# Kernel optimization log

Hardware: AMD Instinct MI355X
Metric: run time of the kernel (lower is better)

## Reference

```python
import jax, jax.numpy as jnp
import numpy as np

B, T, C, NH = 4, 2048, 1024, 16
HS = C // NH  # 64


def setup_inputs() -> dict:
    key = jax.random.key(0)
    ks = jax.random.split(key, 3)
    x = jax.random.normal(ks[0], (B, T, C), dtype=jnp.float32)
    w_attn = jax.random.normal(ks[1], (C, 3 * C), dtype=jnp.float32) * (1.0 / np.sqrt(C))
    b_attn = jnp.zeros((3 * C,), dtype=jnp.float32)
    w_proj = jax.random.normal(ks[2], (C, C), dtype=jnp.float32) * (1.0 / np.sqrt(C))
    b_proj = jnp.zeros((C,), dtype=jnp.float32)
    return {"x": x, "w_attn": w_attn, "b_attn": b_attn, "w_proj": w_proj, "b_proj": b_proj}


def reference(x, w_attn, b_attn, w_proj, b_proj):
    Bx, Tx, Cx = x.shape
    qkv = x @ w_attn + b_attn                      # (B,T,3C)
    q, k, v = jnp.split(qkv, 3, axis=2)
    # faithful to torch: view(B,T,hs,nh).transpose(1,3) -> (B,nh,hs,T)
    def to_heads(t):
        return jnp.transpose(t.reshape(Bx, Tx, HS, NH), (0, 3, 2, 1))
    q, k, v = to_heads(q), to_heads(k), to_heads(v)
    # att[b,h,i,j] = q_i . k_j / sqrt(hs)
    att = jnp.einsum('bhdi,bhdj->bhij', q, k) * (1.0 / np.sqrt(HS))
    # buffer is tril.T == upper-triangular; keep i<=j, mask i>j
    keep = jnp.triu(jnp.ones((Tx, Tx), dtype=bool))[None, None]
    att = jnp.where(keep, att, -jnp.inf)
    att = jax.nn.softmax(att, axis=-2)             # normalize over i
    y = jnp.einsum('bhdi,bhij->bhdj', v, att)      # (B,nh,hs,T)
    y = jnp.transpose(y, (0, 3, 2, 1)).reshape(Bx, Tx, Cx)
    return y @ w_proj + b_proj
```

## Files before the change

kernel.cpp:

```cpp
#include <hip/hip_runtime.h>
#include <stdint.h>


typedef __attribute__((ext_vector_type(8))) _Float16 f16x8;
typedef __attribute__((ext_vector_type(4))) _Float16 f16x4;
typedef __attribute__((ext_vector_type(2))) _Float16 h2;
typedef __attribute__((ext_vector_type(2))) __fp16   fp16x2_t;
typedef __attribute__((ext_vector_type(4))) float    f32x4;

#define NT_   8192
#define NC_   1024
#define N3C_  3072

__device__ __forceinline__ uint32_t pkrtz(float a, float b){
  union { fp16x2_t h; uint32_t u; } cv;
  cv.h = __builtin_amdgcn_cvt_pkrtz(a, b);
  return cv.u;
}

__global__ void k_cvt(const float* __restrict__ src, _Float16* __restrict__ dst, int n4){
  int idx = blockIdx.x*blockDim.x + threadIdx.x;
  int stride = gridDim.x*blockDim.x;
  for (int i = idx; i < n4; i += stride){
    float4 v = ((const float4*)src)[i];
    f16x4 o;
    o[0] = (_Float16)v.x; o[1] = (_Float16)v.y;
    o[2] = (_Float16)v.z; o[3] = (_Float16)v.w;
    ((f16x4*)dst)[i] = o;
  }
}

__global__ void k_wattn_t(const float* __restrict__ w, _Float16* __restrict__ wt){
  int t = threadIdx.x;
  int m0 = blockIdx.x*128, c0 = blockIdx.y*32;
  int mcol = m0 + t;
  int part = mcol >> 10, rr = mcol & 1023;
  int mp = part*1024 + (rr & 15)*64 + (rr >> 4);
  alignas(16) _Float16 buf[32];
  #pragma unroll
  for (int cc = 0; cc < 32; cc++)
    buf[cc] = (_Float16)w[(size_t)(c0+cc)*N3C_ + mcol];
  uint4* dst = (uint4*)(wt + (size_t)mp*NC_ + c0);
  const uint4* sb = (const uint4*)buf;
  dst[0]=sb[0]; dst[1]=sb[1]; dst[2]=sb[2]; dst[3]=sb[3];
}

__global__ void k_wproj_t(const float* __restrict__ w, _Float16* __restrict__ wt){
  int t = threadIdx.x;
  int o0 = blockIdx.x*128, cp0 = blockIdx.y*32;
  int o = o0 + t;
  alignas(16) _Float16 buf[32];
  #pragma unroll
  for (int i = 0; i < 32; i++){
    int cp = cp0 + i;
    int row = (cp & 63)*16 + (cp >> 6);
    buf[i] = (_Float16)w[(size_t)row*NC_ + o];
  }
  uint4* dst = (uint4*)(wt + (size_t)o*NC_ + cp0);
  const uint4* sb = (const uint4*)buf;
  dst[0]=sb[0]; dst[1]=sb[1]; dst[2]=sb[2]; dst[3]=sb[3];
}

__global__ void k_bias(const float* __restrict__ ba, float* __restrict__ bp){
  int i = blockIdx.x*blockDim.x + threadIdx.x;
  int part = i >> 10, rr = i & 1023, h = rr >> 6, d = rr & 63;
  bp[i] = ba[part*1024 + d*16 + h];
}

template<int OUT_HALF>
__global__ __launch_bounds__(256) void k_gemm(
    const _Float16* __restrict__ A, const _Float16* __restrict__ BT,
    const float* __restrict__ bias, void* __restrict__ outp,
    _Float16* __restrict__ VTout,
    int M, int N, int K)
{
  __shared__ _Float16 As[128][40];
  __shared__ _Float16 Bs[128][40];
  int tid = threadIdx.x;
  int wave = tid >> 6, lane = tid & 63;
  int wr = wave >> 1, wc = wave & 1;
  int g = lane >> 4, l15 = lane & 15;
  f32x4 acc[4][4] = {};
  const _Float16* Ag = A  + (size_t)blockIdx.y*128*K;
  const _Float16* Bg = BT + (size_t)blockIdx.x*128*K;
  int srow = tid >> 1, skoff = (tid & 1)*16;
  const _Float16* apt = Ag + (size_t)srow*K + skoff;
  const _Float16* bpt = Bg + (size_t)srow*K + skoff;
  uint4 ra0 = *(const uint4*)apt;
  uint4 ra1 = *(const uint4*)(apt + 8);
  uint4 rb0 = *(const uint4*)bpt;
  uint4 rb1 = *(const uint4*)(bpt + 8);
  for (int kt = 0; kt < K; kt += 32){
    __syncthreads();
    *(uint4*)&As[srow][skoff]     = ra0;
    *(uint4*)&As[srow][skoff + 8] = ra1;
    *(uint4*)&Bs[srow][skoff]     = rb0;
    *(uint4*)&Bs[srow][skoff + 8] = rb1;
    __syncthreads();
    if (kt + 32 < K){
      ra0 = *(const uint4*)(apt + kt + 32);
      ra1 = *(const uint4*)(apt + kt + 40);
      rb0 = *(const uint4*)(bpt + kt + 32);
      rb1 = *(const uint4*)(bpt + kt + 40);
    }
    f16x8 af[4], bf[4];
    #pragma unroll
    for (int mi = 0; mi < 4; mi++) af[mi] = *(const f16x8*)&As[wr*64 + mi*16 + l15][g*8];
    #pragma unroll
    for (int ni = 0; ni < 4; ni++) bf[ni] = *(const f16x8*)&Bs[wc*64 + ni*16 + l15][g*8];
    #pragma unroll
    for (int mi = 0; mi < 4; mi++)
      #pragma unroll
      for (int ni = 0; ni < 4; ni++)
        acc[mi][ni] = __builtin_amdgcn_mfma_f32_16x16x32_f16(af[mi], bf[ni], acc[mi][ni], 0, 0, 0);
  }
  int rowBase = blockIdx.y*128 + wr*64;
  int colBase = blockIdx.x*128 + wc*64;
  if (OUT_HALF && colBase >= 2048){
    int b = rowBase >> 11;
    int t0 = (rowBase & 2047);
    #pragma unroll
    for (int mi = 0; mi < 4; mi++){
      #pragma unroll
      for (int ni = 0; ni < 4; ni++){
        int col = colBase + ni*16 + l15;
        int cc = col - 2048;
        int h = cc >> 6, d = cc & 63;
        float bv = bias[col];
        _Float16* dst = VTout + (((size_t)(b*16 + h)*64 + d)*2048) + t0 + mi*16 + g*4;
        f16x4 o;
        #pragma unroll
        for (int r = 0; r < 4; r++) o[r] = (_Float16)(acc[mi][ni][r] + bv);
        *(f16x4*)dst = o;
      }
    }
    return;
  }
  #pragma unroll
  for (int mi = 0; mi < 4; mi++){
    #pragma unroll
    for (int ni = 0; ni < 4; ni++){
      int col = colBase + ni*16 + l15;
      float bv = bias[col];
      #pragma unroll
      for (int r = 0; r < 4; r++){
        int row = rowBase + mi*16 + g*4 + r;
        float v = acc[mi][ni][r] + bv;
        if (OUT_HALF) ((_Float16*)outp)[(size_t)row*N + col] = (_Float16)v;
        else          ((float*)outp)[(size_t)row*N + col] = v;
      }
    }
  }
}

__global__ __launch_bounds__(256) void k_attn(
    const _Float16* __restrict__ qkv, const _Float16* __restrict__ VTb,
    _Float16* __restrict__ Y)
{
  __shared__ _Float16 Ks[64][72];
  __shared__ _Float16 Vs[64][72];
  __shared__ uint32_t Ps[4][16][32];
  int bid = blockIdx.x;
  int bh = bid & 63;
  int jtA = bid >> 6;
  int jtB = 31 - jtA;
  int b = bh >> 4, h = bh & 15;
  int tid = threadIdx.x, wave = tid >> 6, lane = tid & 63;
  int g = lane >> 4, l15 = lane & 15;
  uint32_t* Pw = &Ps[wave][0][0] + l15*32;
  int xm = (l15 & 7) << 2;
  const _Float16 QS = (_Float16)0.18033688f;

  int q0A = jtA*64 + wave*16, q0B = jtB*64 + wave*16;
  const _Float16* qA = qkv + (size_t)(b*2048 + q0A + l15)*N3C_ + 1024 + h*64;
  const _Float16* qB = qkv + (size_t)(b*2048 + q0B + l15)*N3C_ + 1024 + h*64;
  f16x8 qA0 = *(const f16x8*)&qA[g*8] * QS, qA1 = *(const f16x8*)&qA[32 + g*8] * QS;
  f16x8 qB0 = *(const f16x8*)&qB[g*8] * QS, qB1 = *(const f16x8*)&qB[32 + g*8] * QS;
  float mA = -3e30f, lA = 0.f, mB = -3e30f, lB = 0.f;
  f32x4 accA[4] = {}; f32x4 accB[4] = {};

  int srow = tid >> 2, soff = (tid & 3)*16;
  const _Float16* kbase = qkv + (size_t)(b*2048 + srow)*N3C_ + h*64 + soff;
  const _Float16* vbase = VTb + ((size_t)bh*64 + srow)*2048 + soff;

  auto process = [&](const f16x8& qf0, const f16x8& qf1, float& mrun, float& lrun,
                     f32x4* acc, int q0, int i0, bool diag){
    f32x4 s2[4];
    #pragma unroll
    for (int nb = 0; nb < 4; nb++){
      f16x8 kf0 = *(const f16x8*)&Ks[nb*16 + l15][g*8];
      f16x8 kf1 = *(const f16x8*)&Ks[nb*16 + l15][32 + g*8];
      f32x4 z = {};
      z = __builtin_amdgcn_mfma_f32_16x16x32_f16(kf0, qf0, z, 0, 0, 0);
      z = __builtin_amdgcn_mfma_f32_16x16x32_f16(kf1, qf1, z, 0, 0, 0);
      s2[nb] = z;
    }
    float p[16];
    #pragma unroll
    for (int nb = 0; nb < 4; nb++)
      #pragma unroll
      for (int r = 0; r < 4; r++)
        p[nb*4 + r] = s2[nb][r];
    if (diag){
      int qidx = q0 + l15;
      #pragma unroll
      for (int nb = 0; nb < 4; nb++)
        #pragma unroll
        for (int r = 0; r < 4; r++){
          int kidx = i0 + nb*16 + g*4 + r;
          if (kidx > qidx) p[nb*4 + r] = -3e30f;
        }
    }
    float t0 = fmaxf(fmaxf(p[0],  p[1]),  p[2]);
    float t1 = fmaxf(fmaxf(p[3],  p[4]),  p[5]);
    float t2 = fmaxf(fmaxf(p[6],  p[7]),  p[8]);
    float t3 = fmaxf(fmaxf(p[9],  p[10]), p[11]);
    float t4 = fmaxf(fmaxf(p[12], p[13]), p[14]);
    float mx = fmaxf(fmaxf(fmaxf(t0, t1), t2), fmaxf(fmaxf(t3, t4), p[15]));
    mx = fmaxf(mx, __shfl_xor(mx, 16));
    mx = fmaxf(mx, __shfl_xor(mx, 32));
    float mnew = mrun;
    if (!__all(mx - mrun <= 11.5f)){
      mnew = fmaxf(mrun, mx);
      float alpha = __builtin_amdgcn_exp2f(mrun - mnew);
      lrun *= alpha;
      #pragma unroll
      for (int db = 0; db < 4; db++) acc[db] *= alpha;
    }
    uint32_t pk[8];
    #pragma unroll
    for (int i = 0; i < 8; i++){
      float e0 = __builtin_amdgcn_exp2f(p[2*i]     - mnew);
      float e1 = __builtin_amdgcn_exp2f(p[2*i + 1] - mnew);
      pk[i] = pkrtz(e0, e1);
    }
    const h2 ones = { (_Float16)1.0f, (_Float16)1.0f };
    union { uint32_t u; h2 h; } cv;
    float rs0 = 0.f, rs1 = 0.f;
    #pragma unroll
    for (int i = 0; i < 4; i++){
      cv.u = pk[i];     rs0 = __builtin_amdgcn_fdot2(cv.h, ones, rs0, false);
      cv.u = pk[i + 4]; rs1 = __builtin_amdgcn_fdot2(cv.h, ones, rs1, false);
    }
    float rs = rs0 + rs1;
    rs += __shfl_xor(rs, 16);
    rs += __shfl_xor(rs, 32);
    lrun += rs;
    mrun = mnew;
    #pragma unroll
    for (int nb = 0; nb < 4; nb++)
      #pragma unroll
      for (int r2 = 0; r2 < 2; r2++)
        Pw[(nb*8 + g*2 + r2) ^ xm] = pk[nb*2 + r2];
    #pragma unroll
    for (int ks = 0; ks < 2; ks++){
      f16x8 pb = *(const f16x8*)&Pw[(ks*16 + g*4) ^ xm];
      #pragma unroll
      for (int db = 0; db < 4; db++){
        f16x8 vb = *(const f16x8*)&Vs[db*16 + l15][ks*32 + g*8];
        acc[db] = __builtin_amdgcn_mfma_f32_16x16x32_f16(vb, pb, acc[db], 0, 0, 0);
      }
    }
  };

  uint4 ka0 = *(const uint4*)&kbase[0];
  uint4 ka1 = *(const uint4*)&kbase[8];
  uint4 va0 = *(const uint4*)&vbase[0];
  uint4 va1 = *(const uint4*)&vbase[8];
  for (int it = 0; it <= jtB; ++it){
    __syncthreads();
    *(uint4*)&Ks[srow][soff]     = ka0;
    *(uint4*)&Ks[srow][soff + 8] = ka1;
    *(uint4*)&Vs[srow][soff]     = va0;
    *(uint4*)&Vs[srow][soff + 8] = va1;
    if (it < jtB){
      size_t ko = (size_t)(it+1)*64*N3C_;
      int    vo = (it+1)*64;
      ka0 = *(const uint4*)&kbase[ko];
      ka1 = *(const uint4*)&kbase[ko + 8];
      va0 = *(const uint4*)&vbase[vo];
      va1 = *(const uint4*)&vbase[vo + 8];
    }
    __syncthreads();
    process(qB0, qB1, mB, lB, accB, q0B, it*64, it == jtB);
    if (it <= jtA) process(qA0, qA1, mA, lA, accA, q0A, it*64, it == jtA);
  }

  auto finish = [&](float lr, f32x4* acc, int q0){
    float inv = 1.0f / lr;
    _Float16* yb = Y + (size_t)(b*2048 + q0 + l15)*NC_ + h*64 + g*4;
    #pragma unroll
    for (int db = 0; db < 4; db++){
      f16x4 o;
      #pragma unroll
      for (int r = 0; r < 4; r++) o[r] = (_Float16)(acc[db][r]*inv);
      *(f16x4*)&yb[db*16] = o;
    }
  };
  finish(lA, accA, q0A);
  finish(lB, accB, q0B);
}

extern "C" void kernel_launch(void* const* d_in, const int* in_sizes, int n_in,
                              void* d_out, int out_size, void* d_ws, size_t ws_size,
                              hipStream_t stream)
{
  const float* x      = (const float*)d_in[0];
  const float* w_attn = (const float*)d_in[1];
  const float* b_attn = (const float*)d_in[2];
  const float* w_proj = (const float*)d_in[3];
  const float* b_proj = (const float*)d_in[4];
  float* out = (float*)d_out;
  char* ws = (char*)d_ws;
  _Float16* xb   = (_Float16*)(ws + 0);
  _Float16* wT   = (_Float16*)(ws + 16777216);
  _Float16* wpT  = (_Float16*)(ws + 23068672);
  float*    bp   = (float*)   (ws + 25165824);
  _Float16* qkv  = (_Float16*)(ws + 25178112);
  _Float16* VT   = (_Float16*)(ws + 75509760);
  _Float16* Y    = (_Float16*)(ws + 92286976);

  k_cvt<<<2048, 256, 0, stream>>>(x, xb, (NT_*NC_)/4);
  k_wattn_t<<<dim3(24, 32), 128, 0, stream>>>(w_attn, wT);
  k_wproj_t<<<dim3(8, 32), 128, 0, stream>>>(w_proj, wpT);
  k_bias<<<12, 256, 0, stream>>>(b_attn, bp);
  k_gemm<1><<<dim3(24, 64), 256, 0, stream>>>(xb, wT, bp, qkv, VT, NT_, N3C_, NC_);
  k_attn<<<1024, 256, 0, stream>>>(qkv, VT, Y);
  k_gemm<0><<<dim3(8, 64), 256, 0, stream>>>(Y, wpT, b_proj, out, (_Float16*)nullptr, NT_, NC_, NC_);
}
```

Before: 212.2 us.

## Double-buffer K/V LDS tiles with XOR swizzle and speculative softmax exp

The attention kernel now keeps two K/V LDS buffers, so the next tile is staged after compute and only one barrier is needed per iteration instead of two. The padded [64][72] layout is replaced by an unpadded [64][64] layout with an XOR swizzle on 16-byte chunks to avoid bank conflicts. The softmax exponentials are computed speculatively with the old running max and recomputed only when the max grows, and the PV MFMA is issued before the row-sum reduction. LDS use doubles, and the speculative exp path adds work whenever a rescale is triggered.

```diff
diff --git a/kernel.cpp b/kernel.cpp
--- a/kernel.cpp
+++ b/kernel.cpp
@@ -157,8 +157,8 @@
     const _Float16* __restrict__ qkv, const _Float16* __restrict__ VTb,
     _Float16* __restrict__ Y)
 {
-  __shared__ _Float16 Ks[64][72];
-  __shared__ _Float16 Vs[64][72];
+  __shared__ _Float16 Ks[2][64][64];
+  __shared__ _Float16 Vs[2][64][64];
   __shared__ uint32_t Ps[4][16][32];
   int bid = blockIdx.x;
   int bh = bid & 63;
@@ -169,6 +169,7 @@
   int g = lane >> 4, l15 = lane & 15;
   uint32_t* Pw = &Ps[wave][0][0] + l15*32;
   int xm = (l15 & 7) << 2;
+  int swR = (l15 & 7) << 4;
   const _Float16 QS = (_Float16)0.18033688f;
 
   int q0A = jtA*64 + wave*16, q0B = jtB*64 + wave*16;
@@ -179,17 +180,32 @@
   float mA = -3e30f, lA = 0.f, mB = -3e30f, lB = 0.f;
   f32x4 accA[4] = {}; f32x4 accB[4] = {};
 
-  int srow = tid >> 2, soff = (tid & 3)*16;
-  const _Float16* kbase = qkv + (size_t)(b*2048 + srow)*N3C_ + h*64 + soff;
-  const _Float16* vbase = VTb + ((size_t)bh*64 + srow)*2048 + soff;
+  int srow = tid >> 2;
+  int sbyte = (tid & 3)*32;
+  int swW = (srow & 7) << 4;
+  const _Float16* kbase = qkv + (size_t)(b*2048 + srow)*N3C_ + h*64 + (sbyte>>1);
+  const _Float16* vbase = VTb + ((size_t)bh*64 + srow)*2048 + (sbyte>>1);
+
+  auto stage = [&](int buf, const uint4& k0, const uint4& k1,
+                   const uint4& v0, const uint4& v1){
+    char* kw = (char*)&Ks[buf][0][0] + srow*128;
+    char* vw = (char*)&Vs[buf][0][0] + srow*128;
+    *(uint4*)(kw + ( sbyte       ^ swW)) = k0;
+    *(uint4*)(kw + ((sbyte + 16) ^ swW)) = k1;
+    *(uint4*)(vw + ( sbyte       ^ swW)) = v0;
+    *(uint4*)(vw + ((sbyte + 16) ^ swW)) = v1;
+  };
 
   auto process = [&](const f16x8& qf0, const f16x8& qf1, float& mrun, float& lrun,
-                     f32x4* acc, int q0, int i0, bool diag){
+                     f32x4* acc, int q0, int i0, bool diag, int cur){
+    const char* kb = (const char*)&Ks[cur][0][0];
+    const char* vb = (const char*)&Vs[cur][0][0];
     f32x4 s2[4];
     #pragma unroll
     for (int nb = 0; nb < 4; nb++){
-      f16x8 kf0 = *(const f16x8*)&Ks[nb*16 + l15][g*8];
-      f16x8 kf1 = *(const f16x8*)&Ks[nb*16 + l15][32 + g*8];
+      const char* krow = kb + (nb*16 + l15)*128;
+      f16x8 kf0 = *(const f16x8*)(krow + (( g*16)      ^ swR));
+      f16x8 kf1 = *(const f16x8*)(krow + ((64 + g*16)  ^ swR));
       f32x4 z = {};
       z = __builtin_amdgcn_mfma_f32_16x16x32_f16(kf0, qf0, z, 0, 0, 0);
       z = __builtin_amdgcn_mfma_f32_16x16x32_f16(kf1, qf1, z, 0, 0, 0);
@@ -210,6 +226,13 @@
           int kidx = i0 + nb*16 + g*4 + r;
           if (kidx > qidx) p[nb*4 + r] = -3e30f;
         }
+    }
+    uint32_t pk[8];
+    #pragma unroll
+    for (int i = 0; i < 8; i++){
+      float e0 = __builtin_amdgcn_exp2f(p[2*i]     - mrun);
+      float e1 = __builtin_amdgcn_exp2f(p[2*i + 1] - mrun);
+      pk[i] = pkrtz(e0, e1);
     }
     float t0 = fmaxf(fmaxf(p[0],  p[1]),  p[2]);
     float t1 = fmaxf(fmaxf(p[3],  p[4]),  p[5]);
@@ -219,20 +242,34 @@
     float mx = fmaxf(fmaxf(fmaxf(t0, t1), t2), fmaxf(fmaxf(t3, t4), p[15]));
     mx = fmaxf(mx, __shfl_xor(mx, 16));
     mx = fmaxf(mx, __shfl_xor(mx, 32));
-    float mnew = mrun;
     if (!__all(mx - mrun <= 11.5f)){
-      mnew = fmaxf(mrun, mx);
+      float mnew = fmaxf(mrun, mx);
       float alpha = __builtin_amdgcn_exp2f(mrun - mnew);
       lrun *= alpha;
       #pragma unroll
       for (int db = 0; db < 4; db++) acc[db] *= alpha;
-    }
-    uint32_t pk[8];
-    #pragma unroll
-    for (int i = 0; i < 8; i++){
-      float e0 = __builtin_amdgcn_exp2f(p[2*i]     - mnew);
-      float e1 = __builtin_amdgcn_exp2f(p[2*i + 1] - mnew);
-      pk[i] = pkrtz(e0, e1);
+      #pragma unroll
+      for (int i = 0; i < 8; i++){
+        float e0 = __builtin_amdgcn_exp2f(p[2*i]     - mnew);
+        float e1 = __builtin_amdgcn_exp2f(p[2*i + 1] - mnew);
+        pk[i] = pkrtz(e0, e1);
+      }
+      mrun = mnew;
+    }
+    #pragma unroll
+    for (int nb = 0; nb < 4; nb++)
+      #pragma unroll
+      for (int r2 = 0; r2 < 2; r2++)
+        Pw[(nb*8 + g*2 + r2) ^ xm] = pk[nb*2 + r2];
+    #pragma unroll
+    for (int ks = 0; ks < 2; ks++){
+      f16x8 pb = *(const f16x8*)&Pw[(ks*16 + g*4) ^ xm];
+      #pragma unroll
+      for (int db = 0; db < 4; db++){
+        const char* vrow = vb + (db*16 + l15)*128;
+        f16x8 vv = *(const f16x8*)(vrow + ((ks*64 + g*16) ^ swR));
+        acc[db] = __builtin_amdgcn_mfma_f32_16x16x32_f16(vv, pb, acc[db], 0, 0, 0);
+      }
     }
     const h2 ones = { (_Float16)1.0f, (_Float16)1.0f };
     union { uint32_t u; h2 h; } cv;
@@ -246,33 +283,16 @@
     rs += __shfl_xor(rs, 16);
     rs += __shfl_xor(rs, 32);
     lrun += rs;
-    mrun = mnew;
-    #pragma unroll
-    for (int nb = 0; nb < 4; nb++)
-      #pragma unroll
-      for (int r2 = 0; r2 < 2; r2++)
-        Pw[(nb*8 + g*2 + r2) ^ xm] = pk[nb*2 + r2];
-    #pragma unroll
-    for (int ks = 0; ks < 2; ks++){
-      f16x8 pb = *(const f16x8*)&Pw[(ks*16 + g*4) ^ xm];
-      #pragma unroll
-      for (int db = 0; db < 4; db++){
-        f16x8 vb = *(const f16x8*)&Vs[db*16 + l15][ks*32 + g*8];
-        acc[db] = __builtin_amdgcn_mfma_f32_16x16x32_f16(vb, pb, acc[db], 0, 0, 0);
-      }
-    }
   };
 
   uint4 ka0 = *(const uint4*)&kbase[0];
   uint4 ka1 = *(const uint4*)&kbase[8];
   uint4 va0 = *(const uint4*)&vbase[0];
   uint4 va1 = *(const uint4*)&vbase[8];
+  stage(0, ka0, ka1, va0, va1);
+  __syncthreads();
   for (int it = 0; it <= jtB; ++it){
-    __syncthreads();
-    *(uint4*)&Ks[srow][soff]     = ka0;
-    *(uint4*)&Ks[srow][soff + 8] = ka1;
-    *(uint4*)&Vs[srow][soff]     = va0;
-    *(uint4*)&Vs[srow][soff + 8] = va1;
+    int cur = it & 1;
     if (it < jtB){
       size_t ko = (size_t)(it+1)*64*N3C_;
       int    vo = (it+1)*64;
@@ -281,9 +301,10 @@
       va0 = *(const uint4*)&vbase[vo];
       va1 = *(const uint4*)&vbase[vo + 8];
     }
+    process(qB0, qB1, mB, lB, accB, q0B, it*64, it == jtB, cur);
+    if (it <= jtA) process(qA0, qA1, mA, lA, accA, q0A, it*64, it == jtA, cur);
+    if (it < jtB) stage(cur ^ 1, ka0, ka1, va0, va1);
     __syncthreads();
-    process(qB0, qB1, mB, lB, accB, q0B, it*64, it == jtB);
-    if (it <= jtA) process(qA0, qA1, mA, lA, accA, q0A, it*64, it == jtA);
   }
 
   auto finish = [&](float lr, f32x4* acc, int q0){
```

Result: faster. 208.0 us (-2.0%).
